# Optimization experiments

Hardware: AMD Instinct MI355X
Metric: run time of the kernel (lower is better)

Reference implementation:

```python
import jax, jax.numpy as jnp
import numpy as np
import math

HIDDEN = 2048
NUM_HEADS = 16
HEAD_DIM = HIDDEN // NUM_HEADS
B, S = 2, 2048


def setup_inputs() -> dict:
    key = jax.random.key(0)
    k1, k2, k3, k4, k5 = jax.random.split(key, 5)
    scale = 1.0 / math.sqrt(HIDDEN)
    return {
        "hidden_states": jax.random.normal(k1, (B, S, HIDDEN), dtype=jnp.float32),
        "attention_mask": jnp.ones((B, S), dtype=jnp.float32),
        "Wq": jax.random.normal(k2, (HIDDEN, HIDDEN), dtype=jnp.float32) * scale,
        "Wk": jax.random.normal(k3, (HEAD_DIM, HIDDEN), dtype=jnp.float32) * scale,
        "Wv": jax.random.normal(k4, (HEAD_DIM, HIDDEN), dtype=jnp.float32) * scale,
        "Wo": jax.random.normal(k5, (HIDDEN, HIDDEN), dtype=jnp.float32) * scale,
    }


def reference(hidden_states, attention_mask, Wq, Wk, Wv, Wo):
    bsz, tgt, _ = hidden_states.shape
    # projections (torch Linear: x @ W.T)
    q = (hidden_states @ Wq.T).reshape(bsz, tgt, NUM_HEADS, HEAD_DIM).transpose(0, 2, 1, 3)  # [B,H,S,D]
    k = (hidden_states @ Wk.T)[:, None, :, :]  # [B,1,S,D] (MQA single KV head)
    v = (hidden_states @ Wv.T)[:, None, :, :]
    # scores with MQA broadcast (no K expand materialization)
    scores = jnp.einsum("bhsd,bokd->bhsk", q, k) / math.sqrt(HEAD_DIM)  # [B,H,S,S]
    neg = jnp.finfo(scores.dtype).min
    scores = scores + (1.0 - attention_mask)[:, None, None, :] * neg
    probs = jax.nn.softmax(scores, axis=-1)
    attn = jnp.einsum("bhsk,bokd->bhsd", probs, v)  # [B,H,S,D]
    out = attn.transpose(0, 2, 1, 3).reshape(bsz, tgt, HIDDEN) @ Wo.T
    # cache returned by the module (expanded to all heads, as in torch code)
    key_states = jnp.broadcast_to(k, (bsz, NUM_HEADS, tgt, HEAD_DIM))
    value_states = jnp.broadcast_to(v, (bsz, NUM_HEADS, tgt, HEAD_DIM))
    return out, key_states, value_states
```

## Files before the change

### kernel.cpp

```cpp
#include <hip/hip_runtime.h>
#include <hip/hip_bf16.h>
#include <math.h>

#define B_   2
#define S_   2048
#define HID  2048
#define NH   16
#define HD   128

typedef __bf16 bf16_t;
typedef __bf16 bf16x4 __attribute__((ext_vector_type(4)));
typedef __bf16 bf16x8 __attribute__((ext_vector_type(8)));
typedef float  f32x4  __attribute__((ext_vector_type(4)));
typedef unsigned int u32x4 __attribute__((ext_vector_type(4)));

__device__ __forceinline__ f32x4 mfma16(bf16x8 a, bf16x8 b, f32x4 c) {
    return __builtin_amdgcn_mfma_f32_16x16x32_bf16(a, b, c, 0, 0, 0);
}

__device__ __forceinline__ void gl2lds16(const void* g, void* l) {
    __builtin_amdgcn_global_load_lds((__attribute__((address_space(1))) void*)(g),
                                     (__attribute__((address_space(3))) void*)(l),
                                     16, 0, 0);
}

__device__ __forceinline__ unsigned int pkbf(float a, float b) {
    unsigned short ua = __builtin_bit_cast(unsigned short, (bf16_t)a);
    unsigned short ub = __builtin_bit_cast(unsigned short, (bf16_t)b);
    return (unsigned int)ua | ((unsigned int)ub << 16);
}

__global__ void convert_bf16(const float* __restrict__ s0, const float* __restrict__ s1,
                             const float* __restrict__ s2, const float* __restrict__ s3,
                             const float* __restrict__ s4,
                             bf16_t* __restrict__ d0, bf16_t* __restrict__ d1,
                             bf16_t* __restrict__ d2, bf16_t* __restrict__ d3,
                             bf16_t* __restrict__ d4)
{
    const size_t stride = (size_t)gridDim.x * blockDim.x;
    for (size_t i = (size_t)blockIdx.x * blockDim.x + threadIdx.x; i < 4325376; i += stride) {
        const float* s; bf16_t* d; size_t off;
        if (i < 2097152)      { s = s0; d = d0; off = i; }
        else if (i < 3145728) { s = s1; d = d1; off = i - 2097152; }
        else if (i < 3211264) { s = s2; d = d2; off = i - 3145728; }
        else if (i < 3276800) { s = s3; d = d3; off = i - 3211264; }
        else                  { s = s4; d = d4; off = i - 3276800; }
        float4 v = ((const float4*)s)[off];
        bf16x4 o;
        o[0] = (bf16_t)v.x; o[1] = (bf16_t)v.y; o[2] = (bf16_t)v.z; o[3] = (bf16_t)v.w;
        ((bf16x4*)d)[off] = o;
    }
}

__global__ void broadcast_kv(const bf16_t* __restrict__ k_ws, const bf16_t* __restrict__ v_ws,
                             float* __restrict__ keyo, float* __restrict__ valo)
{
    const size_t stride = (size_t)gridDim.x * blockDim.x;
    for (size_t i = (size_t)blockIdx.x * blockDim.x + threadIdx.x; i < 4194304; i += stride) {
        int which = i >= 2097152;
        size_t f = which ? i - 2097152 : i;
        size_t e = f * 4;
        int d = (int)(e & 127);
        size_t s = (e >> 7) & 2047;
        size_t b = e >> 22;
        const bf16_t* src = (which ? v_ws : k_ws) + (b * S_ + s) * HD + d;
        bf16x4 kv = *(const bf16x4*)src;
        float4 o;
        o.x = (float)kv[0]; o.y = (float)kv[1]; o.z = (float)kv[2]; o.w = (float)kv[3];
        *(float4*)((which ? valo : keyo) + e) = o;
    }
}

template <int MODE>
__global__ __launch_bounds__(256, 2)
void gemm_nt(const bf16_t* __restrict__ A,  const bf16_t* __restrict__ B0,
             const bf16_t* __restrict__ B1, const bf16_t* __restrict__ B2,
             bf16_t* __restrict__ q_ws, bf16_t* __restrict__ k_ws,
             bf16_t* __restrict__ v_ws, bf16_t* __restrict__ vt_ws,
             float* __restrict__ outf)
{
    __shared__ __align__(16) ushort sA[128 * 32];
    __shared__ __align__(16) ushort sB[128 * 32];

    const int tid  = threadIdx.x;
    const int lane = tid & 63;
    const int wave = tid >> 6;
    const int quad = lane >> 4;
    const int l16  = lane & 15;
    const int bn = blockIdx.x, bm = blockIdx.y;
    const int wm = (wave & 1) * 64;
    const int wn = (wave >> 1) * 64;

    const bf16_t* Bbase;
    if (MODE == 0) Bbase = (bn < 16) ? (B0 + (size_t)bn * 128 * HID) : (bn == 16 ? B1 : B2);
    else           Bbase = B0 + (size_t)bn * 128 * HID;
    const bf16_t* Abase = A + (size_t)bm * 128 * HID;

    const int c0 = tid, c1 = tid + 256;
    const int r0 = c0 >> 2, o0 = (c0 & 3) * 8;
    const int r1 = c1 >> 2, o1 = (c1 & 3) * 8;

    f32x4 acc[4][4] = {};

    for (int kt = 0; kt < HID / 32; ++kt) {
        const int ko = kt * 32;
        gl2lds16(Abase + (size_t)r0 * HID + ko + o0, sA + c0 * 8);
        gl2lds16(Abase + (size_t)r1 * HID + ko + o1, sA + c1 * 8);
        gl2lds16(Bbase + (size_t)r0 * HID + ko + o0, sB + c0 * 8);
        gl2lds16(Bbase + (size_t)r1 * HID + ko + o1, sB + c1 * 8);
        __syncthreads();

        bf16x8 af[4], bfr[4];
        for (int mt = 0; mt < 4; ++mt)
            af[mt] = *(const bf16x8*)(sA + (wm + mt * 16 + l16) * 32 + quad * 8);
        for (int nt = 0; nt < 4; ++nt)
            bfr[nt] = *(const bf16x8*)(sB + (wn + nt * 16 + l16) * 32 + quad * 8);
        for (int mt = 0; mt < 4; ++mt)
            for (int nt = 0; nt < 4; ++nt)
                acc[mt][nt] = mfma16(af[mt], bfr[nt], acc[mt][nt]);
        __syncthreads();
    }

    for (int mt = 0; mt < 4; ++mt) {
        for (int nt = 0; nt < 4; ++nt) {
            for (int j = 0; j < 4; ++j) {
                float v = acc[mt][nt][j];
                int row = bm * 128 + wm + mt * 16 + quad * 4 + j;
                int col = wn + nt * 16 + l16;
                if (MODE == 1) {
                    outf[(size_t)row * HID + bn * 128 + col] = v;
                } else {
                    bf16_t bv = (bf16_t)v;
                    if (bn < 16) {
                        q_ws[(size_t)row * HID + bn * 128 + col] = bv;
                    } else {
                        int b = row >> 11, s = row & 2047, d = col;
                        if (bn == 16) {
                            k_ws[((size_t)b * S_ + s) * HD + d] = bv;
                        } else {
                            v_ws[((size_t)b * S_ + s) * HD + d] = bv;
                            vt_ws[((size_t)b * HD + d) * S_ + s] = bv;
                        }
                    }
                }
            }
        }
    }
}

#define KBUF0 0
#define VBUF0 8192
#define KBUF1 16384
#define VBUF1 24576
#define MADD  32768

__global__ __launch_bounds__(256, 2)
void attn_kernel(const bf16_t* __restrict__ Qw, const bf16_t* __restrict__ Kc,
                 const bf16_t* __restrict__ Vt, const float* __restrict__ mask,
                 bf16_t* __restrict__ Ow)
{
    __shared__ __align__(16) ushort smem[36864];
    float* sMadd = (float*)&smem[MADD];

    const int tid  = threadIdx.x;
    const int lane = tid & 63;
    const int wave = tid >> 6;
    const int quad = lane >> 4;
    const int l16  = lane & 15;
    const int qt = blockIdx.x;
    const int bh = blockIdx.y;
    const int b = bh >> 4, h = bh & 15;

    const bf16_t* kg = Kc + (size_t)b * S_ * HD;
    const bf16_t* vg = Vt + (size_t)b * HD * S_;
    const float*  mg = mask + (size_t)b * S_;

    auto STAGE = [&](int t, int kofs, int vofs) {
        const bf16_t* kb = kg + (size_t)t * 64 * HD;
        const bf16_t* vb = vg + t * 64;
#pragma unroll
        for (int i = 0; i < 4; ++i) {
            int c = tid + i * 256;
            int kr = c >> 4, kc = c & 15;
            gl2lds16(kb + (size_t)kr * HD + ((kc ^ (kr & 7)) << 3),
                     &smem[kofs + c * 8]);
            int vr = c >> 3, vc = c & 7;
            gl2lds16(vb + (size_t)vr * S_ + ((vc ^ (vr & 7)) << 3),
                     &smem[vofs + c * 8]);
        }
    };

    bf16x8 qf[2][4];
    {
        const bf16_t* qg = Qw + ((size_t)(b * S_ + qt * 128 + wave * 32)) * HID + h * HD;
#pragma unroll
        for (int mt = 0; mt < 2; ++mt)
#pragma unroll
            for (int kk = 0; kk < 4; ++kk)
                qf[mt][kk] = *(const bf16x8*)(qg + (size_t)(mt * 16 + l16) * HID + kk * 32 + quad * 8);
    }

    f32x4 oa[2][8] = {};
    float mrow[2] = { -INFINITY, -INFINITY };
    float lrow[2] = { 0.f, 0.f };

    const float scale2 = 0.08838834764831845f * 1.4426950408889634f;
    const float NEGF   = -3.4028234663852886e38f;
    const float LOG2E  = 1.4426950408889634f;

#pragma unroll
    for (int i = 0; i < 8; ++i) {
        int idx = tid + i * 256;
        sMadd[idx] = (1.0f - mg[idx]) * NEGF * LOG2E;
    }
    STAGE(0, KBUF0, VBUF0);
    __syncthreads();

    auto body = [&](int t, int kcur, int vcur, int knxt, int vnxt) {
        if (t + 1 < S_ / 64) STAGE(t + 1, knxt, vnxt);

        f32x4 sa[2][4] = {};
#pragma unroll
        for (int kk = 0; kk < 4; ++kk)
#pragma unroll
            for (int nt = 0; nt < 4; ++nt) {
                bf16x8 kf = *(const bf16x8*)(&smem[kcur + (nt * 16 + l16) * 128 + (((4 * kk + quad) ^ (l16 & 7)) << 3)]);
#pragma unroll
                for (int mt = 0; mt < 2; ++mt)
                    sa[mt][nt] = mfma16(kf, qf[mt][kk], sa[mt][nt]);
            }
#pragma unroll
        for (int nt = 0; nt < 4; ++nt) {
            f32x4 m4 = *(const f32x4*)&sMadd[t * 64 + nt * 16 + quad * 4];
#pragma unroll
            for (int mt = 0; mt < 2; ++mt)
#pragma unroll
                for (int j = 0; j < 4; ++j)
                    sa[mt][nt][j] = sa[mt][nt][j] * scale2 + m4[j];
        }

        float rm[2];
#pragma unroll
        for (int mt = 0; mt < 2; ++mt) {
            float m = sa[mt][0][0];
#pragma unroll
            for (int nt = 0; nt < 4; ++nt)
#pragma unroll
                for (int j = 0; j < 4; ++j)
                    m = fmaxf(m, sa[mt][nt][j]);
            m = fmaxf(m, __shfl_xor(m, 16));
            m = fmaxf(m, __shfl_xor(m, 32));
            rm[mt] = m;
        }
        bool need = (rm[0] > mrow[0] + 8.0f) || (rm[1] > mrow[1] + 8.0f);
        if (__any((int)need)) {
#pragma unroll
            for (int mt = 0; mt < 2; ++mt) {
                float mnew  = fmaxf(mrow[mt], rm[mt]);
                float alpha = exp2f(mrow[mt] - mnew);
                mrow[mt] = mnew;
                lrow[mt] *= alpha;
#pragma unroll
                for (int j = 0; j < 4; ++j) {
                    float aj = __shfl(alpha, (lane & 48) | (quad * 4 + j));
#pragma unroll
                    for (int nt = 0; nt < 8; ++nt) oa[mt][nt][j] *= aj;
                }
            }
        }
        unsigned int g[2][4][2];
#pragma unroll
        for (int mt = 0; mt < 2; ++mt) {
            float rs = 0.f;
#pragma unroll
            for (int nt = 0; nt < 4; ++nt) {
                float p0 = exp2f(sa[mt][nt][0] - mrow[mt]);
                float p1 = exp2f(sa[mt][nt][1] - mrow[mt]);
                float p2 = exp2f(sa[mt][nt][2] - mrow[mt]);
                float p3 = exp2f(sa[mt][nt][3] - mrow[mt]);
                rs += (p0 + p1) + (p2 + p3);
                g[mt][nt][0] = pkbf(p0, p1);
                g[mt][nt][1] = pkbf(p2, p3);
            }
            rs += __shfl_xor(rs, 16);
            rs += __shfl_xor(rs, 32);
            lrow[mt] += rs;
        }

        bf16x8 pf[2][2];
        {
            const int sl = ((quad & 1) << 5) + l16;
            const int sh = sl + 16;
            const bool hi = (quad & 2) != 0;
#pragma unroll
            for (int kk = 0; kk < 2; ++kk)
#pragma unroll
                for (int mt = 0; mt < 2; ++mt) {
                    unsigned int a0 = __shfl(g[mt][2 * kk][0], sl);
                    unsigned int a1 = __shfl(g[mt][2 * kk][1], sl);
                    unsigned int b0 = __shfl(g[mt][2 * kk + 1][0], sl);
                    unsigned int b1 = __shfl(g[mt][2 * kk + 1][1], sl);
                    unsigned int c0 = __shfl(g[mt][2 * kk][0], sh);
                    unsigned int c1 = __shfl(g[mt][2 * kk][1], sh);
                    unsigned int d0 = __shfl(g[mt][2 * kk + 1][0], sh);
                    unsigned int d1 = __shfl(g[mt][2 * kk + 1][1], sh);
                    u32x4 w;
                    w[0] = hi ? b0 : a0;
                    w[1] = hi ? b1 : a1;
                    w[2] = hi ? d0 : c0;
                    w[3] = hi ? d1 : c1;
                    pf[mt][kk] = __builtin_bit_cast(bf16x8, w);
                }
        }

#pragma unroll
        for (int kk = 0; kk < 2; ++kk)
#pragma unroll
            for (int nt = 0; nt < 8; ++nt) {
                bf16x8 vf = *(const bf16x8*)(&smem[vcur + (nt * 16 + l16) * 64 + (((4 * kk + quad) ^ (l16 & 7)) << 3)]);
#pragma unroll
                for (int mt = 0; mt < 2; ++mt)
                    oa[mt][nt] = mfma16(pf[mt][kk], vf, oa[mt][nt]);
            }

        __syncthreads();
    };

    for (int kt = 0; kt < S_ / 64; kt += 2) {
        body(kt,     KBUF0, VBUF0, KBUF1, VBUF1);
        body(kt + 1, KBUF1, VBUF1, KBUF0, VBUF0);
    }

#pragma unroll
    for (int mt = 0; mt < 2; ++mt)
#pragma unroll
        for (int j = 0; j < 4; ++j) {
            float lv = __shfl(lrow[mt], (lane & 48) | (quad * 4 + j));
            float inv = 1.0f / lv;
            int s = qt * 128 + wave * 32 + mt * 16 + quad * 4 + j;
#pragma unroll
            for (int nt = 0; nt < 8; ++nt) {
                int d = nt * 16 + l16;
                Ow[((size_t)(b * S_ + s)) * HID + h * HD + d] = (bf16_t)(oa[mt][nt][j] * inv);
            }
        }
}

extern "C" void kernel_launch(void* const* d_in, const int* in_sizes, int n_in,
                              void* d_out, int out_size, void* d_ws, size_t ws_size,
                              hipStream_t stream) {
    const float* hs   = (const float*)d_in[0];
    const float* mask = (const float*)d_in[1];
    const float* Wq   = (const float*)d_in[2];
    const float* Wk   = (const float*)d_in[3];
    const float* Wv   = (const float*)d_in[4];
    const float* Wo   = (const float*)d_in[5];
    float* out = (float*)d_out;

    bf16_t* wqb = (bf16_t*)out;
    bf16_t* wkb = wqb + 4194304;
    bf16_t* wvb = wkb + 262144;
    bf16_t* qb  = (bf16_t*)(out + 8388608);
    bf16_t* wob = (bf16_t*)(out + 12582912);
    bf16_t* hsb = (bf16_t*)(out + 16777216);
    bf16_t* o_ws = hsb;

    bf16_t* k_ws  = (bf16_t*)d_ws;
    bf16_t* v_ws  = k_ws + 524288;
    bf16_t* vt_ws = v_ws + 524288;

    convert_bf16<<<2048, 256, 0, stream>>>(hs, Wq, Wk, Wv, Wo, hsb, wqb, wkb, wvb, wob);
    gemm_nt<0><<<dim3(18, 32), 256, 0, stream>>>(hsb, wqb, wkb, wvb, qb, k_ws, v_ws, vt_ws, nullptr);
    attn_kernel<<<dim3(16, 32), 256, 0, stream>>>(qb, k_ws, vt_ws, mask, o_ws);
    gemm_nt<1><<<dim3(16, 32), 256, 0, stream>>>(o_ws, wob, nullptr, nullptr, nullptr, nullptr, nullptr, nullptr, out);
    broadcast_kv<<<4096, 256, 0, stream>>>(k_ws, v_ws, out + 8388608, out + 16777216);
}
```

Baseline: 381.1 us.

## Double-buffer GEMM LDS tiles and raise wave priority around attention MFMAs

The projection GEMM now uses two LDS buffers, so the global-to-LDS load of the next K tile is issued before the current tile's MFMAs run, removing one barrier per step. Launch bounds go from 2 to 4 blocks per CU, which pushes register allocation down. In the attention kernel, s_setprio brackets the QK and PV MFMA loops so compute waves get issue priority over the softmax phase. The costs are doubled LDS per block and possible register spills under the tighter launch bound.

```diff
diff --git a/kernel.cpp b/kernel.cpp
--- a/kernel.cpp
+++ b/kernel.cpp
@@ -72,15 +72,15 @@
 }
 
 template <int MODE>
-__global__ __launch_bounds__(256, 2)
+__global__ __launch_bounds__(256, 4)
 void gemm_nt(const bf16_t* __restrict__ A,  const bf16_t* __restrict__ B0,
              const bf16_t* __restrict__ B1, const bf16_t* __restrict__ B2,
              bf16_t* __restrict__ q_ws, bf16_t* __restrict__ k_ws,
              bf16_t* __restrict__ v_ws, bf16_t* __restrict__ vt_ws,
              float* __restrict__ outf)
 {
-    __shared__ __align__(16) ushort sA[128 * 32];
-    __shared__ __align__(16) ushort sB[128 * 32];
+    __shared__ __align__(16) ushort sA[2][128 * 32];
+    __shared__ __align__(16) ushort sB[2][128 * 32];
 
     const int tid  = threadIdx.x;
     const int lane = tid & 63;
@@ -102,22 +102,36 @@
 
     f32x4 acc[4][4] = {};
 
-    for (int kt = 0; kt < HID / 32; ++kt) {
+    auto STAGE = [&](int kt, int bi) {
         const int ko = kt * 32;
-        gl2lds16(Abase + (size_t)r0 * HID + ko + o0, sA + c0 * 8);
-        gl2lds16(Abase + (size_t)r1 * HID + ko + o1, sA + c1 * 8);
-        gl2lds16(Bbase + (size_t)r0 * HID + ko + o0, sB + c0 * 8);
-        gl2lds16(Bbase + (size_t)r1 * HID + ko + o1, sB + c1 * 8);
-        __syncthreads();
-
+        gl2lds16(Abase + (size_t)r0 * HID + ko + o0, sA[bi] + c0 * 8);
+        gl2lds16(Abase + (size_t)r1 * HID + ko + o1, sA[bi] + c1 * 8);
+        gl2lds16(Bbase + (size_t)r0 * HID + ko + o0, sB[bi] + c0 * 8);
+        gl2lds16(Bbase + (size_t)r1 * HID + ko + o1, sB[bi] + c1 * 8);
+    };
+    auto COMPUTE = [&](int bi) {
         bf16x8 af[4], bfr[4];
+#pragma unroll
         for (int mt = 0; mt < 4; ++mt)
-            af[mt] = *(const bf16x8*)(sA + (wm + mt * 16 + l16) * 32 + quad * 8);
+            af[mt] = *(const bf16x8*)(sA[bi] + (wm + mt * 16 + l16) * 32 + quad * 8);
+#pragma unroll
         for (int nt = 0; nt < 4; ++nt)
-            bfr[nt] = *(const bf16x8*)(sB + (wn + nt * 16 + l16) * 32 + quad * 8);
+            bfr[nt] = *(const bf16x8*)(sB[bi] + (wn + nt * 16 + l16) * 32 + quad * 8);
+#pragma unroll
         for (int mt = 0; mt < 4; ++mt)
+#pragma unroll
             for (int nt = 0; nt < 4; ++nt)
                 acc[mt][nt] = mfma16(af[mt], bfr[nt], acc[mt][nt]);
+    };
+
+    STAGE(0, 0);
+    __syncthreads();
+    for (int kt = 0; kt < HID / 32; kt += 2) {
+        if (kt + 1 < HID / 32) STAGE(kt + 1, 1);
+        COMPUTE(0);
+        __syncthreads();
+        if (kt + 2 < HID / 32) STAGE(kt + 2, 0);
+        COMPUTE(1);
         __syncthreads();
     }
 
@@ -220,6 +234,7 @@
         if (t + 1 < S_ / 64) STAGE(t + 1, knxt, vnxt);
 
         f32x4 sa[2][4] = {};
+        __builtin_amdgcn_s_setprio(1);
 #pragma unroll
         for (int kk = 0; kk < 4; ++kk)
 #pragma unroll
@@ -229,6 +244,7 @@
                 for (int mt = 0; mt < 2; ++mt)
                     sa[mt][nt] = mfma16(kf, qf[mt][kk], sa[mt][nt]);
             }
+        __builtin_amdgcn_s_setprio(0);
 #pragma unroll
         for (int nt = 0; nt < 4; ++nt) {
             f32x4 m4 = *(const f32x4*)&sMadd[t * 64 + nt * 16 + quad * 4];
@@ -313,6 +329,7 @@
                 }
         }
 
+        __builtin_amdgcn_s_setprio(1);
 #pragma unroll
         for (int kk = 0; kk < 2; ++kk)
 #pragma unroll
@@ -322,6 +339,7 @@
                 for (int mt = 0; mt < 2; ++mt)
                     oa[mt][nt] = mfma16(pf[mt][kk], vf, oa[mt][nt]);
             }
+        __builtin_amdgcn_s_setprio(0);
 
         __syncthreads();
     };
```

Result: no change. 383.1 us (+0.5%).
